# Performance work log

Hardware: AMD Instinct MI355X
Metric: run time of the kernel (lower is better)

The kernel has to match this reference:

```python
import jax, jax.numpy as jnp
import numpy as np

N_NODES = 100000
N_EDGES = 1600000
D_IN = 128
D_OUT = 128
KEEP_PROB = 0.5  # torch code: p_drop = 1 - self.dropout, dropout=0.5


def setup_inputs() -> dict:
    key = jax.random.key(0)
    k1, k2, k3, k4, k5 = jax.random.split(key, 5)
    x = jax.random.normal(k1, (N_NODES, D_IN), dtype=jnp.float32)
    # Glorot uniform init matching weight_variable_glorot
    init_range = np.sqrt(6.0 / (D_IN + D_OUT))
    W = jax.random.uniform(k2, (D_IN, D_OUT), dtype=jnp.float32,
                           minval=-init_range, maxval=init_range)
    adj_row = jax.random.randint(k3, (N_EDGES,), 0, N_NODES, dtype=jnp.int32)
    adj_col = jax.random.randint(k4, (N_EDGES,), 0, N_NODES, dtype=jnp.int32)
    adj_val = jax.random.uniform(k5, (N_EDGES,), dtype=jnp.float32)
    return {"x": x, "W": W, "adj_row": adj_row, "adj_col": adj_col, "adj_val": adj_val}


def reference(x, W, adj_row, adj_col, adj_val):
    # dropout (always training=True in the torch module), deterministic key
    mask = jax.random.bernoulli(jax.random.key(42), KEEP_PROB, x.shape)
    x = jnp.where(mask, x / KEEP_PROB, 0.0)
    # dense GEMM: [N, D_in] @ [D_in, D_out]
    h = x @ W
    # sparse adjacency SpMM in COO form: out[r] += val * h[c]
    msg = adj_val[:, None] * h[adj_col]            # [E, D_out]
    agg = jax.ops.segment_sum(msg, adj_row, num_segments=N_NODES)
    return jax.nn.relu(agg)
```

## Files before the change

### kernel.cpp

```cpp
#include <hip/hip_runtime.h>
#include <hip/hip_bf16.h>

#define N_NODES 100000
#define N_EDGES 1600000
#define D 128
#define NBUCKETS 391
#define BUCKET_EDGES 4096
#define NBLK1 391
#define HCAP 2432

typedef float          floatx4 __attribute__((ext_vector_type(4)));
typedef __bf16         bf16x8  __attribute__((ext_vector_type(8)));
typedef unsigned short ushort8 __attribute__((ext_vector_type(8)));

__device__ __forceinline__ unsigned rotl32(unsigned x, int d) {
    return (x << d) | (x >> (32 - d));
}

__device__ __forceinline__ void threefry_0_42(unsigned c0, unsigned c1,
                                              unsigned& o0, unsigned& o1) {
    const unsigned k0 = 0u, k1 = 42u;
    const unsigned k2 = 0x1BD11BDAu ^ k0 ^ k1;
    unsigned x0 = c0 + k0;
    unsigned x1 = c1 + k1;
#define TF_R4(r0, r1, r2, r3)                      \
    x0 += x1; x1 = rotl32(x1, r0); x1 ^= x0;       \
    x0 += x1; x1 = rotl32(x1, r1); x1 ^= x0;       \
    x0 += x1; x1 = rotl32(x1, r2); x1 ^= x0;       \
    x0 += x1; x1 = rotl32(x1, r3); x1 ^= x0;
    TF_R4(13, 15, 26, 6);  x0 += k1; x1 += k2 + 1u;
    TF_R4(17, 29, 16, 24); x0 += k2; x1 += k0 + 2u;
    TF_R4(13, 15, 26, 6);  x0 += k0; x1 += k1 + 3u;
    TF_R4(17, 29, 16, 24); x0 += k1; x1 += k2 + 4u;
    TF_R4(13, 15, 26, 6);  x0 += k2; x1 += k0 + 5u;
#undef TF_R4
    o0 = x0; o1 = x1;
}

__device__ __forceinline__ bool keep_elem(unsigned i) {
    unsigned o0, o1;
    threefry_0_42(0u, i, o0, o1);
    return (((o0 ^ o1) >> 31) == 0u);
}

__device__ __forceinline__ unsigned short f32_bf16(float f) {
    unsigned u = __float_as_uint(f);
    u += 0x7fffu + ((u >> 16) & 1u);
    return (unsigned short)(u >> 16);
}

__global__ __launch_bounds__(256)
void k_gemm(const float* __restrict__ x, const float* __restrict__ W,
            unsigned short* __restrict__ hb) {
    __shared__ __align__(16) unsigned short Wt[128][136];
    __shared__ __align__(16) unsigned short xs[32][136];

    const int t = threadIdx.x;
    const int g = blockIdx.x;

    {
        int n      = t & 127;
        int k8base = t >> 7;
#pragma unroll
        for (int it = 0; it < 8; ++it) {
            int k8 = (it * 2 + k8base) * 8;
            unsigned short tmp[8];
#pragma unroll
            for (int j = 0; j < 8; ++j)
                tmp[j] = f32_bf16(W[(k8 + j) * 128 + n]);
            *(ushort8*)&Wt[n][k8] = *(ushort8*)tmp;
        }
    }
    {
        int m  = t >> 4;
        int c0 = (t & 15) * 8;
        int r0 = g * 32 + m;
        const float* pa = x + r0 * D + c0;
        const float* pb = x + (r0 + 16) * D + c0;
        float va[8], vb[8];
        *(float4*)&va[0] = ((const float4*)pa)[0];
        *(float4*)&va[4] = ((const float4*)pa)[1];
        *(float4*)&vb[0] = ((const float4*)pb)[0];
        *(float4*)&vb[4] = ((const float4*)pb)[1];
        int ibase = r0 * D + c0;
        unsigned short ta[8], tb[8];
#pragma unroll
        for (int j = 0; j < 8; ++j) {
            float fa = keep_elem((unsigned)(ibase + j))        ? 2.0f * va[j] : 0.0f;
            float fb = keep_elem((unsigned)(ibase + 2048 + j)) ? 2.0f * vb[j] : 0.0f;
            ta[j] = f32_bf16(fa);
            tb[j] = f32_bf16(fb);
        }
        *(ushort8*)&xs[m][c0]      = *(ushort8*)ta;
        *(ushort8*)&xs[16 + m][c0] = *(ushort8*)tb;
    }
    __syncthreads();

    const int w  = t >> 6;
    const int l  = t & 63;
    const int rt = w >> 1;
    const int ctbase = (w & 1) * 4;
    const int mm = l & 15;
    const int q  = l >> 4;
    const int koff = q * 8;
    const unsigned short* xrow = &xs[rt * 16 + mm][0];
    const int growbase = g * 32 + rt * 16;

    for (int ci = 0; ci < 4; ++ci) {
        int ct = ctbase + ci;
        const unsigned short* wrow = &Wt[ct * 16 + mm][0];
        floatx4 acc = {0.f, 0.f, 0.f, 0.f};
#pragma unroll
        for (int kt = 0; kt < 4; ++kt) {
            bf16x8 a = *(const bf16x8*)(xrow + kt * 32 + koff);
            bf16x8 b = *(const bf16x8*)(wrow + kt * 32 + koff);
            acc = __builtin_amdgcn_mfma_f32_16x16x32_bf16(a, b, acc, 0, 0, 0);
        }
        int col = ct * 16 + mm;
#pragma unroll
        for (int reg = 0; reg < 4; ++reg) {
            int grow = growbase + q * 4 + reg;
            hb[grow * D + col] = f32_bf16(acc[reg]);
        }
    }
}

__global__ __launch_bounds__(256)
void k_bhist(const int* __restrict__ row, int* __restrict__ bcnt) {
    __shared__ int h[NBUCKETS];
    const int t = threadIdx.x;
    for (int i = t; i < NBUCKETS; i += 256) h[i] = 0;
    __syncthreads();
    int base = blockIdx.x * BUCKET_EDGES;
#pragma unroll
    for (int k = 0; k < 4; ++k) {
        int e4 = base + (k * 256 + t) * 4;
        if (e4 < N_EDGES) {
            int4 r = *(const int4*)(row + e4);
            atomicAdd(&h[r.x >> 8], 1);
            atomicAdd(&h[r.y >> 8], 1);
            atomicAdd(&h[r.z >> 8], 1);
            atomicAdd(&h[r.w >> 8], 1);
        }
    }
    __syncthreads();
    for (int i = t; i < NBUCKETS; i += 256)
        if (h[i]) atomicAdd(&bcnt[i], h[i]);
}

__global__ __launch_bounds__(512)
void k_bscan(const int* __restrict__ bcnt, int* __restrict__ bstart,
             int* __restrict__ bcur) {
    __shared__ int s[512];
    int t = threadIdx.x;
    int v = (t < NBUCKETS) ? bcnt[t] : 0;
    s[t] = v;
    __syncthreads();
    for (int off = 1; off < 512; off <<= 1) {
        int a = (t >= off) ? s[t - off] : 0;
        __syncthreads();
        s[t] += a;
        __syncthreads();
    }
    if (t < NBUCKETS) {
        int st = s[t] - v;
        bstart[t] = st;
        bcur[t]   = st;
    }
    if (t == 0) bstart[NBUCKETS] = N_EDGES;
}

__global__ __launch_bounds__(256)
void k_bucket(const int* __restrict__ row, const int* __restrict__ col,
              const float* __restrict__ val, int* __restrict__ bcur,
              int2* __restrict__ buf) {
    __shared__ int h[NBUCKETS];
    __shared__ int lbase[NBUCKETS];
    const int t = threadIdx.x;
    for (int i = t; i < NBUCKETS; i += 256) h[i] = 0;
    __syncthreads();

    int rows[16], cols[16];
    float vals[16];
    int base = blockIdx.x * BUCKET_EDGES;
#pragma unroll
    for (int k = 0; k < 4; ++k) {
        int e4 = base + (k * 256 + t) * 4;
        if (e4 < N_EDGES) {
            *(int4*)&rows[k * 4]   = *(const int4*)(row + e4);
            *(int4*)&cols[k * 4]   = *(const int4*)(col + e4);
            *(float4*)&vals[k * 4] = *(const float4*)(val + e4);
        } else {
            rows[k * 4] = rows[k * 4 + 1] = rows[k * 4 + 2] = rows[k * 4 + 3] = -1;
        }
    }
#pragma unroll
    for (int j = 0; j < 16; ++j)
        if (rows[j] >= 0) atomicAdd(&h[rows[j] >> 8], 1);
    __syncthreads();

    for (int i = t; i < NBUCKETS; i += 256) {
        int c = h[i];
        lbase[i] = c ? atomicAdd(&bcur[i], c) : 0;
    }
    __syncthreads();
    for (int i = t; i < NBUCKETS; i += 256) h[i] = 0;
    __syncthreads();

#pragma unroll
    for (int j = 0; j < 16; ++j) {
        if (rows[j] >= 0) {
            int bb = rows[j] >> 8;
            int pos = lbase[bb] + atomicAdd(&h[bb], 1);
            int2 ent;
            ent.x = cols[j] | ((rows[j] & 255) << 17);
            ent.y = __float_as_int(vals[j]);
            buf[pos] = ent;
        }
    }
}

__global__ __launch_bounds__(512)
void k_sortgather(const int* __restrict__ bstart, const int2* __restrict__ buf,
                  const unsigned short* __restrict__ hb, float* __restrict__ out) {
    __shared__ __align__(16) int2 ents[HCAP];
    __shared__ __align__(16) int2 ents2[HCAP];
    __shared__ int cnt_[128];
    __shared__ int scan_[128];
    __shared__ int cur_[128];
    __shared__ int nkeep;

    const int b = blockIdx.x, t = threadIdx.x;
    const int bucket = b >> 1;
    const int rbase  = (b & 1) << 7;
    const int s0 = bstart[bucket];
    const int n  = bstart[bucket + 1] - s0;

    if (t < 128) cnt_[t] = 0;
    if (t == 0)  nkeep = 0;
    __syncthreads();

    for (int i = t; i < n; i += 512) {
        int2 e = buf[s0 + i];
        int rl = (e.x >> 17) - rbase;
        if ((unsigned)rl < 128u) {
            int p = atomicAdd(&nkeep, 1);
            ents[p] = e;
            atomicAdd(&cnt_[rl], 1);
        }
    }
    __syncthreads();

    if (t < 128) scan_[t] = cnt_[t];
    __syncthreads();
    for (int off = 1; off < 128; off <<= 1) {
        int a = 0;
        if (t < 128 && t >= off) a = scan_[t - off];
        __syncthreads();
        if (t < 128) scan_[t] += a;
        __syncthreads();
    }
    if (t < 128) cur_[t] = scan_[t] - cnt_[t];
    __syncthreads();

    int nk = nkeep;
    for (int p = t; p < nk; p += 512) {
        int2 e = ents[p];
        int rl = (e.x >> 17) - rbase;
        int pos = atomicAdd(&cur_[rl], 1);
        ents2[pos] = e;
    }
    __syncthreads();

    const int w  = t >> 6;
    const int l2 = (t & 63) * 2;
    const unsigned short* hbl = hb + l2;
    for (int r = 0; r < 16; ++r) {
        int rl = w * 16 + r;
        int c  = cnt_[rl];
        int b0 = scan_[rl] - c;
        float a0 = 0.f, a1 = 0.f;
        int i = 0;
        for (; i + 8 <= c; i += 8) {
            int2 e[8];
#pragma unroll
            for (int j = 0; j < 8; ++j) e[j] = ents2[b0 + i + j];
            unsigned hv[8];
#pragma unroll
            for (int j = 0; j < 8; ++j)
                hv[j] = *(const unsigned*)(hbl + (e[j].x & 0x1FFFF) * D);
#pragma unroll
            for (int j = 0; j < 8; ++j) {
                float v = __int_as_float(e[j].y);
                a0 = fmaf(v, __uint_as_float(hv[j] << 16), a0);
                a1 = fmaf(v, __uint_as_float(hv[j] & 0xffff0000u), a1);
            }
        }
        for (; i + 4 <= c; i += 4) {
            int2 e[4];
#pragma unroll
            for (int j = 0; j < 4; ++j) e[j] = ents2[b0 + i + j];
            unsigned hv[4];
#pragma unroll
            for (int j = 0; j < 4; ++j)
                hv[j] = *(const unsigned*)(hbl + (e[j].x & 0x1FFFF) * D);
#pragma unroll
            for (int j = 0; j < 4; ++j) {
                float v = __int_as_float(e[j].y);
                a0 = fmaf(v, __uint_as_float(hv[j] << 16), a0);
                a1 = fmaf(v, __uint_as_float(hv[j] & 0xffff0000u), a1);
            }
        }
        for (; i < c; ++i) {
            int2 e = ents2[b0 + i];
            float v = __int_as_float(e.y);
            unsigned hv = *(const unsigned*)(hbl + (e.x & 0x1FFFF) * D);
            a0 = fmaf(v, __uint_as_float(hv << 16), a0);
            a1 = fmaf(v, __uint_as_float(hv & 0xffff0000u), a1);
        }
        int grow = (bucket << 8) + rbase + rl;
        if (grow < N_NODES) {
            float2 rr;
            rr.x = a0 > 0.f ? a0 : 0.f;
            rr.y = a1 > 0.f ? a1 : 0.f;
            *(float2*)(out + grow * D + l2) = rr;
        }
    }
}

extern "C" void kernel_launch(void* const* d_in, const int* in_sizes, int n_in,
                              void* d_out, int out_size, void* d_ws, size_t ws_size,
                              hipStream_t stream) {
    const float* x    = (const float*)d_in[0];
    const float* W    = (const float*)d_in[1];
    const int*   arow = (const int*)d_in[2];
    const int*   acol = (const int*)d_in[3];
    const float* aval = (const float*)d_in[4];
    float* out = (float*)d_out;

    char* ws = (char*)d_ws;
    unsigned short* hb = (unsigned short*)ws;
    size_t off = 25600000;
    int* bcnt   = (int*)(ws + off); off += 1568;
    int* bstart = (int*)(ws + off); off += 1568;
    int* bcur   = (int*)(ws + off); off += 1568;
    int2* buf   = (int2*)(ws + off); off += 12800000;

    hipMemsetAsync(bcnt, 0, 1568, stream);
    k_bhist      <<<NBLK1, 256, 0, stream>>>(arow, bcnt);
    k_bscan      <<<1, 512, 0, stream>>>(bcnt, bstart, bcur);
    k_bucket     <<<NBLK1, 256, 0, stream>>>(arow, acol, aval, bcur, buf);
    k_gemm       <<<3125, 256, 0, stream>>>(x, W, hb);
    k_sortgather <<<2 * NBUCKETS, 512, 0, stream>>>(bstart, buf, hb, out);
}
```

Baseline: 245.9 us.

## Use 32-row buckets so sort-gather blocks need no filtering and less shared memory

The edge bucketing moves from 256-row to 32-row buckets (3125 of them). Each sort-gather block now owns one bucket, holds its edges in registers and does a single counting sort in shared memory with a wavefront shuffle scan. This removes the redundant double read-and-filter and the large shared buffers, which should allow higher occupancy. Column offsets are premultiplied by D in the packed entry, and the gather inner loop is unrolled to 16. Risks: histogram and bucket kernels now touch 3125 shared counters and many more global atomics on bcur. A bucket holding more than 768 edges (HCAP 720) would overflow, though with uniform random rows the mean is 512.

After: 259.3 us. 1.05x slower.

```diff
diff --git a/kernel.cpp b/kernel.cpp
--- a/kernel.cpp
+++ b/kernel.cpp
@@ -4,10 +4,10 @@
 #define N_NODES 100000
 #define N_EDGES 1600000
 #define D 128
-#define NBUCKETS 391
+#define NBUCKETS 3125
 #define BUCKET_EDGES 4096
 #define NBLK1 391
-#define HCAP 2432
+#define HCAP 720
 
 typedef float          floatx4 __attribute__((ext_vector_type(4)));
 typedef __bf16         bf16x8  __attribute__((ext_vector_type(8)));
@@ -137,10 +137,10 @@
         int e4 = base + (k * 256 + t) * 4;
         if (e4 < N_EDGES) {
             int4 r = *(const int4*)(row + e4);
-            atomicAdd(&h[r.x >> 8], 1);
-            atomicAdd(&h[r.y >> 8], 1);
-            atomicAdd(&h[r.z >> 8], 1);
-            atomicAdd(&h[r.w >> 8], 1);
+            atomicAdd(&h[r.x >> 5], 1);
+            atomicAdd(&h[r.y >> 5], 1);
+            atomicAdd(&h[r.z >> 5], 1);
+            atomicAdd(&h[r.w >> 5], 1);
         }
     }
     __syncthreads();
@@ -148,24 +148,37 @@
         if (h[i]) atomicAdd(&bcnt[i], h[i]);
 }
 
-__global__ __launch_bounds__(512)
+__global__ __launch_bounds__(1024)
 void k_bscan(const int* __restrict__ bcnt, int* __restrict__ bstart,
              int* __restrict__ bcur) {
-    __shared__ int s[512];
-    int t = threadIdx.x;
-    int v = (t < NBUCKETS) ? bcnt[t] : 0;
-    s[t] = v;
-    __syncthreads();
-    for (int off = 1; off < 512; off <<= 1) {
+    __shared__ int s[1024];
+    const int t = threadIdx.x;
+    const int base = t * 4;
+    int v[4];
+    int sum = 0;
+#pragma unroll
+    for (int j = 0; j < 4; ++j) {
+        int idx = base + j;
+        v[j] = (idx < NBUCKETS) ? bcnt[idx] : 0;
+        sum += v[j];
+    }
+    s[t] = sum;
+    __syncthreads();
+    for (int off = 1; off < 1024; off <<= 1) {
         int a = (t >= off) ? s[t - off] : 0;
         __syncthreads();
         s[t] += a;
         __syncthreads();
     }
-    if (t < NBUCKETS) {
-        int st = s[t] - v;
-        bstart[t] = st;
-        bcur[t]   = st;
+    int run = (t > 0) ? s[t - 1] : 0;
+#pragma unroll
+    for (int j = 0; j < 4; ++j) {
+        int idx = base + j;
+        if (idx < NBUCKETS) {
+            bstart[idx] = run;
+            bcur[idx]   = run;
+        }
+        run += v[j];
     }
     if (t == 0) bstart[NBUCKETS] = N_EDGES;
 }
@@ -196,7 +209,7 @@
     }
 #pragma unroll
     for (int j = 0; j < 16; ++j)
-        if (rows[j] >= 0) atomicAdd(&h[rows[j] >> 8], 1);
+        if (rows[j] >= 0) atomicAdd(&h[rows[j] >> 5], 1);
     __syncthreads();
 
     for (int i = t; i < NBUCKETS; i += 256) {
@@ -210,121 +223,127 @@
 #pragma unroll
     for (int j = 0; j < 16; ++j) {
         if (rows[j] >= 0) {
-            int bb = rows[j] >> 8;
+            int bb = rows[j] >> 5;
             int pos = lbase[bb] + atomicAdd(&h[bb], 1);
             int2 ent;
-            ent.x = cols[j] | ((rows[j] & 255) << 17);
+            ent.x = (cols[j] << 7) | ((rows[j] & 31) << 24);
             ent.y = __float_as_int(vals[j]);
             buf[pos] = ent;
         }
     }
 }
 
-__global__ __launch_bounds__(512)
+__global__ __launch_bounds__(256, 6)
 void k_sortgather(const int* __restrict__ bstart, const int2* __restrict__ buf,
                   const unsigned short* __restrict__ hb, float* __restrict__ out) {
-    __shared__ __align__(16) int2 ents[HCAP];
     __shared__ __align__(16) int2 ents2[HCAP];
-    __shared__ int cnt_[128];
-    __shared__ int scan_[128];
-    __shared__ int cur_[128];
-    __shared__ int nkeep;
+    __shared__ int cnt_[32];
+    __shared__ int scan_[32];
+    __shared__ int cur_[32];
 
     const int b = blockIdx.x, t = threadIdx.x;
-    const int bucket = b >> 1;
-    const int rbase  = (b & 1) << 7;
-    const int s0 = bstart[bucket];
-    const int n  = bstart[bucket + 1] - s0;
-
-    if (t < 128) cnt_[t] = 0;
-    if (t == 0)  nkeep = 0;
-    __syncthreads();
-
-    for (int i = t; i < n; i += 512) {
-        int2 e = buf[s0 + i];
-        int rl = (e.x >> 17) - rbase;
-        if ((unsigned)rl < 128u) {
-            int p = atomicAdd(&nkeep, 1);
-            ents[p] = e;
-            atomicAdd(&cnt_[rl], 1);
-        }
-    }
-    __syncthreads();
-
-    if (t < 128) scan_[t] = cnt_[t];
-    __syncthreads();
-    for (int off = 1; off < 128; off <<= 1) {
-        int a = 0;
-        if (t < 128 && t >= off) a = scan_[t - off];
-        __syncthreads();
-        if (t < 128) scan_[t] += a;
-        __syncthreads();
-    }
-    if (t < 128) cur_[t] = scan_[t] - cnt_[t];
-    __syncthreads();
-
-    int nk = nkeep;
-    for (int p = t; p < nk; p += 512) {
-        int2 e = ents[p];
-        int rl = (e.x >> 17) - rbase;
-        int pos = atomicAdd(&cur_[rl], 1);
-        ents2[pos] = e;
+    const int s0 = bstart[b];
+    const int n  = bstart[b + 1] - s0;
+
+    if (t < 32) cnt_[t] = 0;
+    __syncthreads();
+
+    int2 er[3];
+    int  rl_[3];
+#pragma unroll
+    for (int k = 0; k < 3; ++k) {
+        int i = k * 256 + t;
+        if (i < n) {
+            er[k]  = buf[s0 + i];
+            rl_[k] = (unsigned)er[k].x >> 24;
+            atomicAdd(&cnt_[rl_[k]], 1);
+        } else {
+            rl_[k] = -1;
+        }
+    }
+    __syncthreads();
+
+    if (t < 32) {
+        int v = cnt_[t];
+        int x = v;
+#pragma unroll
+        for (int off = 1; off < 32; off <<= 1) {
+            int u = __shfl_up(x, off);
+            if (t >= off) x += u;
+        }
+        scan_[t] = x;
+        cur_[t]  = x - v;
+    }
+    __syncthreads();
+
+#pragma unroll
+    for (int k = 0; k < 3; ++k) {
+        if (rl_[k] >= 0) {
+            int pos = atomicAdd(&cur_[rl_[k]], 1);
+            ents2[pos] = er[k];
+        }
     }
     __syncthreads();
 
     const int w  = t >> 6;
     const int l2 = (t & 63) * 2;
     const unsigned short* hbl = hb + l2;
-    for (int r = 0; r < 16; ++r) {
-        int rl = w * 16 + r;
+    for (int r = 0; r < 8; ++r) {
+        int rl = w * 8 + r;
         int c  = cnt_[rl];
         int b0 = scan_[rl] - c;
         float a0 = 0.f, a1 = 0.f;
         int i = 0;
-        for (; i + 8 <= c; i += 8) {
-            int2 e[8];
-#pragma unroll
-            for (int j = 0; j < 8; ++j) e[j] = ents2[b0 + i + j];
-            unsigned hv[8];
-#pragma unroll
-            for (int j = 0; j < 8; ++j)
-                hv[j] = *(const unsigned*)(hbl + (e[j].x & 0x1FFFF) * D);
-#pragma unroll
-            for (int j = 0; j < 8; ++j) {
-                float v = __int_as_float(e[j].y);
-                a0 = fmaf(v, __uint_as_float(hv[j] << 16), a0);
-                a1 = fmaf(v, __uint_as_float(hv[j] & 0xffff0000u), a1);
+        for (; i + 16 <= c; i += 16) {
+            unsigned ex[16];
+            float    vv[16];
+#pragma unroll
+            for (int j = 0; j < 16; ++j) {
+                int2 e = ents2[b0 + i + j];
+                ex[j] = (unsigned)e.x & 0xFFFFFFu;
+                vv[j] = __int_as_float(e.y);
             }
+            unsigned hv[16];
+#pragma unroll
+            for (int j = 0; j < 16; ++j)
+                hv[j] = *(const unsigned*)(hbl + ex[j]);
+#pragma unroll
+            for (int j = 0; j < 16; ++j) {
+                a0 = fmaf(vv[j], __uint_as_float(hv[j] << 16), a0);
+                a1 = fmaf(vv[j], __uint_as_float(hv[j] & 0xffff0000u), a1);
+            }
         }
         for (; i + 4 <= c; i += 4) {
-            int2 e[4];
-#pragma unroll
-            for (int j = 0; j < 4; ++j) e[j] = ents2[b0 + i + j];
+            unsigned ex[4];
+            float    vv[4];
+#pragma unroll
+            for (int j = 0; j < 4; ++j) {
+                int2 e = ents2[b0 + i + j];
+                ex[j] = (unsigned)e.x & 0xFFFFFFu;
+                vv[j] = __int_as_float(e.y);
+            }
             unsigned hv[4];
 #pragma unroll
             for (int j = 0; j < 4; ++j)
-                hv[j] = *(const unsigned*)(hbl + (e[j].x & 0x1FFFF) * D);
+                hv[j] = *(const unsigned*)(hbl + ex[j]);
 #pragma unroll
             for (int j = 0; j < 4; ++j) {
-                float v = __int_as_float(e[j].y);
-                a0 = fmaf(v, __uint_as_float(hv[j] << 16), a0);
-                a1 = fmaf(v, __uint_as_float(hv[j] & 0xffff0000u), a1);
+                a0 = fmaf(vv[j], __uint_as_float(hv[j] << 16), a0);
+                a1 = fmaf(vv[j], __uint_as_float(hv[j] & 0xffff0000u), a1);
             }
         }
         for (; i < c; ++i) {
             int2 e = ents2[b0 + i];
             float v = __int_as_float(e.y);
-            unsigned hv = *(const unsigned*)(hbl + (e.x & 0x1FFFF) * D);
+            unsigned hv = *(const unsigned*)(hbl + ((unsigned)e.x & 0xFFFFFFu));
             a0 = fmaf(v, __uint_as_float(hv << 16), a0);
             a1 = fmaf(v, __uint_as_float(hv & 0xffff0000u), a1);
         }
-        int grow = (bucket << 8) + rbase + rl;
-        if (grow < N_NODES) {
-            float2 rr;
-            rr.x = a0 > 0.f ? a0 : 0.f;
-            rr.y = a1 > 0.f ? a1 : 0.f;
-            *(float2*)(out + grow * D + l2) = rr;
-        }
+        int grow = (b << 5) + rl;
+        float2 rr;
+        rr.x = a0 > 0.f ? a0 : 0.f;
+        rr.y = a1 > 0.f ? a1 : 0.f;
+        *(float2*)(out + grow * D + l2) = rr;
     }
 }
 
@@ -341,15 +360,15 @@
     char* ws = (char*)d_ws;
     unsigned short* hb = (unsigned short*)ws;
     size_t off = 25600000;
-    int* bcnt   = (int*)(ws + off); off += 1568;
-    int* bstart = (int*)(ws + off); off += 1568;
-    int* bcur   = (int*)(ws + off); off += 1568;
+    int* bcnt   = (int*)(ws + off); off += 12512;
+    int* bstart = (int*)(ws + off); off += 12512;
+    int* bcur   = (int*)(ws + off); off += 12512;
     int2* buf   = (int2*)(ws + off); off += 12800000;
 
-    hipMemsetAsync(bcnt, 0, 1568, stream);
+    hipMemsetAsync(bcnt, 0, (NBUCKETS + 1) * 4, stream);
     k_bhist      <<<NBLK1, 256, 0, stream>>>(arow, bcnt);
-    k_bscan      <<<1, 512, 0, stream>>>(bcnt, bstart, bcur);
+    k_bscan      <<<1, 1024, 0, stream>>>(bcnt, bstart, bcur);
     k_bucket     <<<NBLK1, 256, 0, stream>>>(arow, acol, aval, bcur, buf);
     k_gemm       <<<3125, 256, 0, stream>>>(x, W, hb);
-    k_sortgather <<<2 * NBUCKETS, 512, 0, stream>>>(bstart, buf, hb, out);
-}
+    k_sortgather <<<NBUCKETS, 256, 0, stream>>>(bstart, buf, hb, out);
+}
```
